# Optimization experiments

Hardware: AMD Instinct MI355X
Metric: run time of the kernel (lower is better)

The kernel has to match this reference:

```python
import jax, jax.numpy as jnp
import numpy as np

N = 100000
E = 1600000
IN_C = 128
OUT_C = 64
EDGE_DIM = 16
EDGE_HID = 32
EPS = 1e-5


def setup_inputs() -> dict:
    key = jax.random.key(0)
    ks = jax.random.split(key, 12)
    x = jax.random.normal(ks[0], (N, IN_C), dtype=jnp.float32)
    edge_index = jax.random.randint(ks[1], (2, E), 0, N, dtype=jnp.int64)
    edge_attr = jax.random.uniform(ks[2], (E, EDGE_DIM), dtype=jnp.float32)
    # PDNConv params
    lin_w = jax.random.normal(ks[3], (OUT_C, IN_C), dtype=jnp.float32) / np.sqrt(IN_C)
    bias = jnp.zeros((OUT_C,), dtype=jnp.float32)
    mlp_w1 = jax.random.normal(ks[4], (EDGE_HID, EDGE_DIM), dtype=jnp.float32) / np.sqrt(EDGE_DIM)
    mlp_b1 = jnp.zeros((EDGE_HID,), dtype=jnp.float32)
    mlp_w2 = jax.random.normal(ks[5], (1, EDGE_HID), dtype=jnp.float32) / np.sqrt(EDGE_HID)
    mlp_b2 = jnp.zeros((1,), dtype=jnp.float32)
    # PReLU (single shared parameter, torch default init 0.25)
    prelu_a = jnp.asarray(0.25, dtype=jnp.float32)
    # GraphNorm params
    gn_weight = jnp.ones((OUT_C,), dtype=jnp.float32)
    gn_bias = jnp.zeros((OUT_C,), dtype=jnp.float32)
    gn_mean_scale = jnp.ones((OUT_C,), dtype=jnp.float32)
    return {
        "x": x, "edge_index": edge_index, "edge_attr": edge_attr,
        "lin_w": lin_w, "bias": bias,
        "mlp_w1": mlp_w1, "mlp_b1": mlp_b1, "mlp_w2": mlp_w2, "mlp_b2": mlp_b2,
        "prelu_a": prelu_a,
        "gn_weight": gn_weight, "gn_bias": gn_bias, "gn_mean_scale": gn_mean_scale,
    }


def reference(x, edge_index, edge_attr, lin_w, bias, mlp_w1, mlp_b1, mlp_w2, mlp_b2,
              prelu_a, gn_weight, gn_bias, gn_mean_scale):
    n = x.shape[0]
    # --- PDNConv ---
    # edge MLP: Linear -> ReLU -> Linear -> Sigmoid -> scalar gate per edge
    h = jax.nn.relu(edge_attr @ mlp_w1.T + mlp_b1)           # [E, hid]
    ew = jax.nn.sigmoid(h @ mlp_w2.T + mlp_b2)[:, 0]         # [E]
    # add self-loops with weight 1.0
    loop = jnp.arange(n)
    row = jnp.concatenate([edge_index[0], loop])             # source
    col = jnp.concatenate([edge_index[1], loop])             # target
    ew = jnp.concatenate([ew, jnp.ones((n,), dtype=x.dtype)])
    # gcn_norm: D^{-1/2} A D^{-1/2} with weighted degree on targets
    deg = jax.ops.segment_sum(ew, col, num_segments=n)       # [N]
    dinv = jnp.where(deg > 0, jax.lax.rsqrt(deg), 0.0)
    norm = dinv[row] * ew * dinv[col]                        # [E+N]
    xt = x @ lin_w.T                                         # [N, out]
    msgs = norm[:, None] * xt[row]                           # gather + gate
    out = jax.ops.segment_sum(msgs, col, num_segments=n) + bias  # scatter-add
    # --- PReLU ---
    out = jnp.where(out >= 0, out, prelu_a * out)
    # --- GraphNorm (single graph) ---
    mean = out.mean(axis=0)                                  # [out]
    centered = out - gn_mean_scale * mean
    var = jnp.mean(centered * centered, axis=0)
    out = gn_weight * centered * jax.lax.rsqrt(var + EPS) + gn_bias
    return out
```

## Files before the change

kernel.cpp:

```cpp
#include <hip/hip_runtime.h>
#include <hip/hip_fp16.h>
#include <math.h>

#define IN_C   128
#define OUT_C  64
#define EDIM   16
#define EHID   32
#define GN_EPS 1e-5f

#define DPAD 3

typedef unsigned long long u64;

__device__ __forceinline__ float dot4(float4 a, float4 b) {
    return a.x * b.x + a.y * b.y + a.z * b.z + a.w * b.w;
}
__device__ __forceinline__ void fma4(float4& a, float s, float4 w) {
    a.x = fmaf(s, w.x, a.x); a.y = fmaf(s, w.y, a.y);
    a.z = fmaf(s, w.z, a.z); a.w = fmaf(s, w.w, a.w);
}
__device__ __forceinline__ float getc(float4 v, int j) {
    return j == 0 ? v.x : j == 1 ? v.y : j == 2 ? v.z : v.w;
}

__global__ void k_init(u64* __restrict__ degcnt, float* __restrict__ sums, int N) {
    int i = blockIdx.x * 256 + threadIdx.x;
    if (i < N) degcnt[(size_t)i << DPAD] = (1ull << 32);
    if (i < 2 * OUT_C) sums[i] = 0.f;
}

__global__ void k_edge(const float* __restrict__ ea, const int* __restrict__ ei,
                       const float* __restrict__ w1, const float* __restrict__ b1,
                       const float* __restrict__ w2, const float* __restrict__ b2,
                       u64* __restrict__ degcnt, int2* __restrict__ tmp, int E) {
    int e = blockIdx.x * 256 + threadIdx.x;
    if (e >= E) return;

    const float4* eav = (const float4*)ea + (size_t)e * 4;
    float4 a0 = eav[0], a1 = eav[1], a2 = eav[2], a3 = eav[3];

    const float4* w1v = (const float4*)w1;
    float z = b2[0];
    #pragma unroll
    for (int j = 0; j < EHID; ++j) {
        float4 q0 = w1v[j * 4 + 0];
        float4 q1 = w1v[j * 4 + 1];
        float4 q2 = w1v[j * 4 + 2];
        float4 q3 = w1v[j * 4 + 3];
        float h = dot4(a0, q0) + dot4(a1, q1) + dot4(a2, q2) + dot4(a3, q3) + b1[j];
        h = fmaxf(h, 0.f);
        z += h * w2[j];
    }
    float ewv = 1.f / (1.f + __expf(-z));

    int row = ei[e];
    int col = ei[E + e];
    u64 inc = (1ull << 44) | (u64)(ewv * 4294967296.0f);
    u64 old = atomicAdd(&degcnt[(size_t)col << DPAD], inc);
    int rank = (int)(old >> 44);
    tmp[e] = make_int2(row | (rank << 17), __float_as_int(ewv));
}

__global__ void k_finish(const u64* __restrict__ degcnt, float* __restrict__ dinv,
                         int* __restrict__ cnt, int N) {
    int i = blockIdx.x * 256 + threadIdx.x;
    if (i < N) {
        u64 v = degcnt[(size_t)i << DPAD];
        float deg = (float)(v & ((1ull << 44) - 1)) * (1.f / 4294967296.f);
        dinv[i] = rsqrtf(deg);
        cnt[i] = (int)(v >> 44);
    }
}

__global__ void k_scan1(const u64* __restrict__ degcnt, int* __restrict__ start,
                        int* __restrict__ bsums, float* __restrict__ dinv,
                        int* __restrict__ cnt, int N) {
    __shared__ int s[256];
    int t = threadIdx.x;
    int i = blockIdx.x * 256 + t;
    int v = 0;
    if (i < N) {
        u64 dv = degcnt[(size_t)i << DPAD];
        v = (int)(dv >> 44);
        float deg = (float)(dv & ((1ull << 44) - 1)) * (1.f / 4294967296.f);
        dinv[i] = rsqrtf(deg);
        cnt[i] = v;
    }
    s[t] = v;
    __syncthreads();
    #pragma unroll
    for (int off = 1; off < 256; off <<= 1) {
        int u = (t >= off) ? s[t - off] : 0;
        __syncthreads();
        s[t] += u;
        __syncthreads();
    }
    if (i < N) start[i] = s[t] - v;
    if (t == 255) bsums[blockIdx.x] = s[255];
}
__global__ void k_scan2(int* __restrict__ bsums, int nb) {
    __shared__ int s[1024];
    int t = threadIdx.x;
    s[t] = (t < nb) ? bsums[t] : 0;
    __syncthreads();
    #pragma unroll
    for (int off = 1; off < 1024; off <<= 1) {
        int u = (t >= off) ? s[t - off] : 0;
        __syncthreads();
        s[t] += u;
        __syncthreads();
    }
    if (t < nb) bsums[t] = (t == 0) ? 0 : s[t - 1];
}

__global__ void k_pass2(const int* __restrict__ ei, const int2* __restrict__ tmp,
                        const int* __restrict__ start, const int* __restrict__ bsums,
                        u64* __restrict__ rec, int E) {
    int e = blockIdx.x * 256 + threadIdx.x;
    if (e >= E) return;
    int col = ei[E + e];
    int2 t = tmp[e];
    int rank = ((unsigned)t.x) >> 17;
    int pos = start[col] + bsums[col >> 8] + rank;
    u64 v = (u64)(unsigned)(t.x & 0x1FFFF) | ((u64)(unsigned)t.y << 32);
    __hip_atomic_store(&rec[pos], v, __ATOMIC_RELAXED, __HIP_MEMORY_SCOPE_AGENT);
}

__global__ void k_xt(const float* __restrict__ x, const float* __restrict__ lw,
                     const float* __restrict__ dinv, __half* __restrict__ xts, int N) {
    __shared__ float swt[IN_C * OUT_C];
    int tid = threadIdx.x;
    for (int i = tid; i < IN_C * OUT_C; i += 256) {
        int k = i >> 6, c = i & 63;
        swt[i] = lw[c * IN_C + k];
    }
    __syncthreads();

    int lane = tid & 63;
    int c4 = lane & 15;
    int rq = lane >> 4;
    int rbase = blockIdx.x * 64 + (tid >> 6) * 16 + rq * 4;

    int r0 = min(rbase + 0, N - 1), r1 = min(rbase + 1, N - 1);
    int r2 = min(rbase + 2, N - 1), r3 = min(rbase + 3, N - 1);
    const float4* x4 = (const float4*)x;
    float4 acc0 = {0,0,0,0}, acc1 = {0,0,0,0}, acc2 = {0,0,0,0}, acc3 = {0,0,0,0};

    #pragma unroll 4
    for (int k4 = 0; k4 < IN_C / 4; ++k4) {
        float4 xv0 = x4[(size_t)r0 * 32 + k4];
        float4 xv1 = x4[(size_t)r1 * 32 + k4];
        float4 xv2 = x4[(size_t)r2 * 32 + k4];
        float4 xv3 = x4[(size_t)r3 * 32 + k4];
        #pragma unroll
        for (int j = 0; j < 4; ++j) {
            float4 wv = *(const float4*)&swt[(k4 * 4 + j) * OUT_C + (c4 << 2)];
            fma4(acc0, getc(xv0, j), wv);
            fma4(acc1, getc(xv1, j), wv);
            fma4(acc2, getc(xv2, j), wv);
            fma4(acc3, getc(xv3, j), wv);
        }
    }
    int cc = c4 << 2;
    #pragma unroll
    for (int i = 0; i < 4; ++i) {
        int r = rbase + i;
        if (r < N) {
            float d = dinv[r];
            float4 a = i == 0 ? acc0 : i == 1 ? acc1 : i == 2 ? acc2 : acc3;
            union { __half2 h[2]; uint2 u; } cv;
            cv.h[0] = __floats2half2_rn(a.x * d, a.y * d);
            cv.h[1] = __floats2half2_rn(a.z * d, a.w * d);
            *(uint2*)&xts[(size_t)r * OUT_C + cc] = cv.u;
        }
    }
}

__global__ void k_gather(const u64* __restrict__ rec, const int* __restrict__ start,
                         const int* __restrict__ bsums, const int* __restrict__ cnt,
                         const float* __restrict__ dinv, const __half* __restrict__ xts,
                         const float* __restrict__ bias, float* __restrict__ out, int N) {
    int node = blockIdx.x * 4 + (threadIdx.x >> 6);
    if (node >= N) return;
    int lane = threadIdx.x & 63;
    int beg = start[node] + bsums[node >> 8];
    int num = cnt[node];
    float acc = __half2float(xts[((size_t)node << 6) + lane]);
    int j = 0;
    for (; j + 8 <= num; j += 8) {
        u64 rc[8];
        #pragma unroll
        for (int u = 0; u < 8; ++u) rc[u] = rec[beg + j + u];
        float v[8];
        #pragma unroll
        for (int u = 0; u < 8; ++u)
            v[u] = __half2float(xts[((size_t)(unsigned)(rc[u] & 0x1FFFF) << 6) + lane]);
        #pragma unroll
        for (int u = 0; u < 8; ++u)
            acc = fmaf(__int_as_float((int)(rc[u] >> 32)), v[u], acc);
    }
    for (; j < num; ++j) {
        u64 rc = rec[beg + j];
        acc = fmaf(__int_as_float((int)(rc >> 32)),
                   __half2float(xts[((size_t)(unsigned)(rc & 0x1FFFF) << 6) + lane]), acc);
    }
    out[((size_t)node << 6) + lane] = bias[lane] + dinv[node] * acc;
}

__global__ void k_init_out(const float* __restrict__ bias, const float* __restrict__ dinv,
                           const __half* __restrict__ xts, float* __restrict__ out, int total) {
    int t = blockIdx.x * 256 + threadIdx.x;
    if (t >= total) return;
    int i = t >> 6, c = t & 63;
    out[t] = bias[c] + dinv[i] * __half2float(xts[t]);
}
__global__ void k_scatter(const int* __restrict__ ei, const int2* __restrict__ tmp,
                          const float* __restrict__ dinv, const __half* __restrict__ xts,
                          float* __restrict__ out, int E) {
    int t = blockIdx.x * 256 + threadIdx.x;
    int e = t >> 6;
    if (e >= E) return;
    int lane = t & 63;
    int2 tm = tmp[e];
    int row = tm.x & 0x1FFFF;
    int col = ei[E + e];
    float w = dinv[col] * __int_as_float(tm.y);
    atomicAdd(out + (size_t)col * OUT_C + lane,
              w * __half2float(xts[(size_t)row * OUT_C + lane]));
}

__global__ void k_stats(const float* __restrict__ out, const float* __restrict__ pa,
                        float* __restrict__ sums, int total) {
    __shared__ float r1[256], r2[256];
    float a = pa[0];
    float s = 0.f, s2 = 0.f;
    int stride = gridDim.x * 256;
    for (int t = blockIdx.x * 256 + threadIdx.x; t < total; t += stride) {
        float v = out[t];
        float y = v >= 0.f ? v : a * v;
        s += y; s2 += y * y;
    }
    int tid = threadIdx.x;
    r1[tid] = s; r2[tid] = s2;
    __syncthreads();
    if (tid < 64) {
        float t1 = r1[tid] + r1[tid + 64] + r1[tid + 128] + r1[tid + 192];
        float t2 = r2[tid] + r2[tid + 64] + r2[tid + 128] + r2[tid + 192];
        atomicAdd(&sums[tid], t1);
        atomicAdd(&sums[OUT_C + tid], t2);
    }
}
__global__ void k_apply(float* __restrict__ out, const float* __restrict__ pa,
                        const float* __restrict__ sums,
                        const float* __restrict__ gw, const float* __restrict__ gb,
                        const float* __restrict__ gms, int total, float invN) {
    int t = blockIdx.x * 256 + threadIdx.x;
    if (t >= total) return;
    int c = t & 63;
    float a  = pa[0];
    float m  = sums[c] * invN;
    float ms = gms[c];
    float var = sums[OUT_C + c] * invN - ms * m * m * (2.f - ms);
    float A = gw[c] * rsqrtf(var + GN_EPS);
    float v = out[t];
    float y = v >= 0.f ? v : a * v;
    out[t] = A * (y - ms * m) + gb[c];
}

extern "C" void kernel_launch(void* const* d_in, const int* in_sizes, int n_in,
                              void* d_out, int out_size, void* d_ws, size_t ws_size,
                              hipStream_t stream) {
    (void)n_in; (void)out_size;
    const float* x    = (const float*)d_in[0];
    const int*   ei   = (const int*)  d_in[1];
    const float* ea   = (const float*)d_in[2];
    const float* lw   = (const float*)d_in[3];
    const float* bias = (const float*)d_in[4];
    const float* w1   = (const float*)d_in[5];
    const float* b1   = (const float*)d_in[6];
    const float* w2   = (const float*)d_in[7];
    const float* b2   = (const float*)d_in[8];
    const float* pa   = (const float*)d_in[9];
    const float* gw   = (const float*)d_in[10];
    const float* gb   = (const float*)d_in[11];
    const float* gms  = (const float*)d_in[12];
    float* out = (float*)d_out;

    int N = in_sizes[0] / IN_C;
    int E = in_sizes[2] / EDIM;
    int total = N * OUT_C;
    int nbN = (N + 255) / 256;
    int nbE = (E + 255) / 256;

    char* p = (char*)d_ws;
    u64*   degcnt = (u64*)p;  p += sizeof(u64) * ((size_t)N << DPAD);
    float* dinv   = (float*)p; p += sizeof(float) * (size_t)N;
    __half* xts   = (__half*)p; p += sizeof(__half) * (size_t)N * OUT_C;
    float* sums   = (float*)p; p += sizeof(float) * 128;
    int*   cnt    = (int*)p;   p += sizeof(int) * (size_t)N;
    int*   startv = (int*)p;   p += sizeof(int) * (size_t)N;
    int*   bsums  = (int*)p;   p += sizeof(int) * 1024;
    int2*  tmp    = (int2*)p;  p += sizeof(int2) * (size_t)E;
    u64*   rec    = (u64*)p;   p += sizeof(u64) * (size_t)E;
    size_t need = (size_t)(p - (char*)d_ws);
    bool use_csr = (need <= ws_size) && (nbN <= 1024);

    k_init <<<nbN, 256, 0, stream>>>(degcnt, sums, N);
    k_edge <<<nbE, 256, 0, stream>>>(ea, ei, w1, b1, w2, b2, degcnt, tmp, E);

    if (use_csr) {
        k_scan1 <<<nbN, 256, 0, stream>>>(degcnt, startv, bsums, dinv, cnt, N);
        k_scan2 <<<1, 1024, 0, stream>>>(bsums, nbN);
        k_pass2 <<<nbE, 256, 0, stream>>>(ei, tmp, startv, bsums, rec, E);
        k_xt    <<<(N + 63) / 64, 256, 0, stream>>>(x, lw, dinv, xts, N);
        k_gather<<<(N + 3) / 4, 256, 0, stream>>>(rec, startv, bsums, cnt, dinv, xts, bias, out, N);
    } else {
        k_finish<<<nbN, 256, 0, stream>>>(degcnt, dinv, cnt, N);
        k_xt    <<<(N + 63) / 64, 256, 0, stream>>>(x, lw, dinv, xts, N);
        k_init_out<<<(total + 255) / 256, 256, 0, stream>>>(bias, dinv, xts, out, total);
        long st = (long)E * 64;
        k_scatter <<<(unsigned)((st + 255) / 256), 256, 0, stream>>>(ei, tmp, dinv, xts, out, E);
    }

    k_stats <<<512, 256, 0, stream>>>(out, pa, sums, total);
    k_apply <<<(total + 255) / 256, 256, 0, stream>>>(out, pa, sums, gw, gb, gms, total,
                                                      1.0f / (float)N);
}
```

Before: 467.2 us.

## Fuse PReLU and GraphNorm statistics into CSR gather kernel; unpad degree counters

The CSR gather kernel becomes grid-stride, applies PReLU, writes the activated output and accumulates per-channel sum and sum-of-squares, which are then atomically added. This removes the separate stats pass, a full re-read of the 25.6MB output, and lets the apply kernel skip PReLU. DPAD drops from 3 to 0, so degree counters are packed rather than spaced out, which shrinks the init and scan footprint but may raise atomic contention between neighbouring counters. Capping the grid at 2048 blocks may reduce latency hiding in the gather.

```diff
diff --git a/kernel.cpp b/kernel.cpp
--- a/kernel.cpp
+++ b/kernel.cpp
@@ -8,7 +8,7 @@
 #define EHID   32
 #define GN_EPS 1e-5f
 
-#define DPAD 3
+#define DPAD 0
 
 typedef unsigned long long u64;
 
@@ -179,32 +179,55 @@
 __global__ void k_gather(const u64* __restrict__ rec, const int* __restrict__ start,
                          const int* __restrict__ bsums, const int* __restrict__ cnt,
                          const float* __restrict__ dinv, const __half* __restrict__ xts,
-                         const float* __restrict__ bias, float* __restrict__ out, int N) {
-    int node = blockIdx.x * 4 + (threadIdx.x >> 6);
-    if (node >= N) return;
-    int lane = threadIdx.x & 63;
-    int beg = start[node] + bsums[node >> 8];
-    int num = cnt[node];
-    float acc = __half2float(xts[((size_t)node << 6) + lane]);
-    int j = 0;
-    for (; j + 8 <= num; j += 8) {
-        u64 rc[8];
-        #pragma unroll
-        for (int u = 0; u < 8; ++u) rc[u] = rec[beg + j + u];
-        float v[8];
-        #pragma unroll
-        for (int u = 0; u < 8; ++u)
-            v[u] = __half2float(xts[((size_t)(unsigned)(rc[u] & 0x1FFFF) << 6) + lane]);
-        #pragma unroll
-        for (int u = 0; u < 8; ++u)
-            acc = fmaf(__int_as_float((int)(rc[u] >> 32)), v[u], acc);
-    }
-    for (; j < num; ++j) {
-        u64 rc = rec[beg + j];
-        acc = fmaf(__int_as_float((int)(rc >> 32)),
-                   __half2float(xts[((size_t)(unsigned)(rc & 0x1FFFF) << 6) + lane]), acc);
-    }
-    out[((size_t)node << 6) + lane] = bias[lane] + dinv[node] * acc;
+                         const float* __restrict__ bias, const float* __restrict__ pa,
+                         float* __restrict__ out, float* __restrict__ sums, int N) {
+    __shared__ float r1[256], r2[256];
+    int tid  = threadIdx.x;
+    int lane = tid & 63;
+    float a = pa[0];
+    float bl = bias[lane];
+    float s = 0.f, s2 = 0.f;
+
+    int ngroups = (N + 3) >> 2;
+    for (int g = blockIdx.x; g < ngroups; g += gridDim.x) {
+        int node = g * 4 + (tid >> 6);
+        if (node < N) {
+            int beg = start[node] + bsums[node >> 8];
+            int num = cnt[node];
+            float acc = __half2float(xts[((size_t)node << 6) + lane]);
+            int j = 0;
+            for (; j + 8 <= num; j += 8) {
+                u64 rc[8];
+                #pragma unroll
+                for (int u = 0; u < 8; ++u) rc[u] = rec[beg + j + u];
+                float v[8];
+                #pragma unroll
+                for (int u = 0; u < 8; ++u)
+                    v[u] = __half2float(xts[((size_t)(unsigned)(rc[u] & 0x1FFFF) << 6) + lane]);
+                #pragma unroll
+                for (int u = 0; u < 8; ++u)
+                    acc = fmaf(__int_as_float((int)(rc[u] >> 32)), v[u], acc);
+            }
+            for (; j < num; ++j) {
+                u64 rc = rec[beg + j];
+                acc = fmaf(__int_as_float((int)(rc >> 32)),
+                           __half2float(xts[((size_t)(unsigned)(rc & 0x1FFFF) << 6) + lane]), acc);
+            }
+            float v = bl + dinv[node] * acc;
+            float y = v >= 0.f ? v : a * v;
+            out[((size_t)node << 6) + lane] = y;
+            s += y; s2 += y * y;
+        }
+    }
+
+    r1[tid] = s; r2[tid] = s2;
+    __syncthreads();
+    if (tid < 64) {
+        float t1 = r1[tid] + r1[tid + 64] + r1[tid + 128] + r1[tid + 192];
+        float t2 = r2[tid] + r2[tid + 64] + r2[tid + 128] + r2[tid + 192];
+        atomicAdd(&sums[tid], t1);
+        atomicAdd(&sums[OUT_C + tid], t2);
+    }
 }
 
 __global__ void k_init_out(const float* __restrict__ bias, const float* __restrict__ dinv,
@@ -228,7 +251,6 @@
     atomicAdd(out + (size_t)col * OUT_C + lane,
               w * __half2float(xts[(size_t)row * OUT_C + lane]));
 }
-
 __global__ void k_stats(const float* __restrict__ out, const float* __restrict__ pa,
                         float* __restrict__ sums, int total) {
     __shared__ float r1[256], r2[256];
@@ -250,10 +272,24 @@
         atomicAdd(&sums[OUT_C + tid], t2);
     }
 }
-__global__ void k_apply(float* __restrict__ out, const float* __restrict__ pa,
-                        const float* __restrict__ sums,
-                        const float* __restrict__ gw, const float* __restrict__ gb,
-                        const float* __restrict__ gms, int total, float invN) {
+
+__global__ void k_apply_csr(float* __restrict__ out, const float* __restrict__ sums,
+                            const float* __restrict__ gw, const float* __restrict__ gb,
+                            const float* __restrict__ gms, int total, float invN) {
+    int t = blockIdx.x * 256 + threadIdx.x;
+    if (t >= total) return;
+    int c = t & 63;
+    float m  = sums[c] * invN;
+    float ms = gms[c];
+    float var = sums[OUT_C + c] * invN - ms * m * m * (2.f - ms);
+    float A = gw[c] * rsqrtf(var + GN_EPS);
+    float y = out[t];
+    out[t] = A * (y - ms * m) + gb[c];
+}
+__global__ void k_apply_fb(float* __restrict__ out, const float* __restrict__ pa,
+                           const float* __restrict__ sums,
+                           const float* __restrict__ gw, const float* __restrict__ gb,
+                           const float* __restrict__ gms, int total, float invN) {
     int t = blockIdx.x * 256 + threadIdx.x;
     if (t >= total) return;
     int c = t & 63;
@@ -309,20 +345,24 @@
     k_edge <<<nbE, 256, 0, stream>>>(ea, ei, w1, b1, w2, b2, degcnt, tmp, E);
 
     if (use_csr) {
+        int ngroups = (N + 3) >> 2;
+        int gblocks = ngroups < 2048 ? ngroups : 2048;
         k_scan1 <<<nbN, 256, 0, stream>>>(degcnt, startv, bsums, dinv, cnt, N);
         k_scan2 <<<1, 1024, 0, stream>>>(bsums, nbN);
         k_pass2 <<<nbE, 256, 0, stream>>>(ei, tmp, startv, bsums, rec, E);
         k_xt    <<<(N + 63) / 64, 256, 0, stream>>>(x, lw, dinv, xts, N);
-        k_gather<<<(N + 3) / 4, 256, 0, stream>>>(rec, startv, bsums, cnt, dinv, xts, bias, out, N);
+        k_gather<<<gblocks, 256, 0, stream>>>(rec, startv, bsums, cnt, dinv, xts,
+                                              bias, pa, out, sums, N);
+        k_apply_csr<<<(total + 255) / 256, 256, 0, stream>>>(out, sums, gw, gb, gms,
+                                                             total, 1.0f / (float)N);
     } else {
         k_finish<<<nbN, 256, 0, stream>>>(degcnt, dinv, cnt, N);
         k_xt    <<<(N + 63) / 64, 256, 0, stream>>>(x, lw, dinv, xts, N);
         k_init_out<<<(total + 255) / 256, 256, 0, stream>>>(bias, dinv, xts, out, total);
         long st = (long)E * 64;
         k_scatter <<<(unsigned)((st + 255) / 256), 256, 0, stream>>>(ei, tmp, dinv, xts, out, E);
-    }
-
-    k_stats <<<512, 256, 0, stream>>>(out, pa, sums, total);
-    k_apply <<<(total + 255) / 256, 256, 0, stream>>>(out, pa, sums, gw, gb, gms, total,
-                                                      1.0f / (float)N);
-}
+        k_stats <<<512, 256, 0, stream>>>(out, pa, sums, total);
+        k_apply_fb<<<(total + 255) / 256, 256, 0, stream>>>(out, pa, sums, gw, gb, gms,
+                                                            total, 1.0f / (float)N);
+    }
+}
```

New measurement: 477.4 us. 2.2% more time.

## Replace scan-based CSR build with fixed-capacity per-node buckets plus overflow list

Applied to the files above, without the earlier changes.

Instead of counting ranks, prefix-scanning degrees and running a second pass to place edge records, each edge now writes its record straight into a per-node bucket of fixed capacity during the edge-MLP kernel, using the atomic rank. Edges past the capacity go to a small overflow list that a separate kernel scatters with atomics. This removes the two scan kernels and the pass2 kernel along with the tmp buffer round trip. The degree counters also lose their padding. The cost is a sparse, larger record array and a correctness risk if the overflow list exceeds its capacity.

```diff
diff --git a/kernel.cpp b/kernel.cpp
--- a/kernel.cpp
+++ b/kernel.cpp
@@ -7,8 +7,8 @@
 #define EDIM   16
 #define EHID   32
 #define GN_EPS 1e-5f
-
-#define DPAD 3
+#define MAXDEG 48
+#define OVFCAP 2048
 
 typedef unsigned long long u64;
 
@@ -23,16 +23,19 @@
     return j == 0 ? v.x : j == 1 ? v.y : j == 2 ? v.z : v.w;
 }
 
-__global__ void k_init(u64* __restrict__ degcnt, float* __restrict__ sums, int N) {
+__global__ void k_init(u64* __restrict__ degcnt, float* __restrict__ sums,
+                       u64* __restrict__ ovfcnt, int N) {
     int i = blockIdx.x * 256 + threadIdx.x;
-    if (i < N) degcnt[(size_t)i << DPAD] = (1ull << 32);
+    if (i < N) degcnt[i] = (1ull << 32);
     if (i < 2 * OUT_C) sums[i] = 0.f;
+    if (i == 0) *ovfcnt = 0ull;
 }
 
 __global__ void k_edge(const float* __restrict__ ea, const int* __restrict__ ei,
                        const float* __restrict__ w1, const float* __restrict__ b1,
                        const float* __restrict__ w2, const float* __restrict__ b2,
-                       u64* __restrict__ degcnt, int2* __restrict__ tmp, int E) {
+                       u64* __restrict__ degcnt, u64* __restrict__ rec,
+                       u64* __restrict__ ovfcnt, int4* __restrict__ ovflist, int E) {
     int e = blockIdx.x * 256 + threadIdx.x;
     if (e >= E) return;
 
@@ -56,7 +59,43 @@
     int row = ei[e];
     int col = ei[E + e];
     u64 inc = (1ull << 44) | (u64)(ewv * 4294967296.0f);
-    u64 old = atomicAdd(&degcnt[(size_t)col << DPAD], inc);
+    u64 old = atomicAdd(&degcnt[col], inc);
+    int rank = (int)(old >> 44);
+    if (rank < MAXDEG) {
+        u64 v = (u64)(unsigned)row | ((u64)(unsigned)__float_as_int(ewv) << 32);
+        __hip_atomic_store(&rec[(size_t)col * MAXDEG + rank], v,
+                           __ATOMIC_RELAXED, __HIP_MEMORY_SCOPE_AGENT);
+    } else {
+        u64 oi = atomicAdd(ovfcnt, 1ull);
+        if (oi < OVFCAP) ovflist[oi] = make_int4(row, col, __float_as_int(ewv), 0);
+    }
+}
+
+__global__ void k_edge_fb(const float* __restrict__ ea, const int* __restrict__ ei,
+                          const float* __restrict__ w1, const float* __restrict__ b1,
+                          const float* __restrict__ w2, const float* __restrict__ b2,
+                          u64* __restrict__ degcnt, int2* __restrict__ tmp, int E) {
+    int e = blockIdx.x * 256 + threadIdx.x;
+    if (e >= E) return;
+    const float4* eav = (const float4*)ea + (size_t)e * 4;
+    float4 a0 = eav[0], a1 = eav[1], a2 = eav[2], a3 = eav[3];
+    const float4* w1v = (const float4*)w1;
+    float z = b2[0];
+    #pragma unroll
+    for (int j = 0; j < EHID; ++j) {
+        float4 q0 = w1v[j * 4 + 0];
+        float4 q1 = w1v[j * 4 + 1];
+        float4 q2 = w1v[j * 4 + 2];
+        float4 q3 = w1v[j * 4 + 3];
+        float h = dot4(a0, q0) + dot4(a1, q1) + dot4(a2, q2) + dot4(a3, q3) + b1[j];
+        h = fmaxf(h, 0.f);
+        z += h * w2[j];
+    }
+    float ewv = 1.f / (1.f + __expf(-z));
+    int row = ei[e];
+    int col = ei[E + e];
+    u64 inc = (1ull << 44) | (u64)(ewv * 4294967296.0f);
+    u64 old = atomicAdd(&degcnt[col], inc);
     int rank = (int)(old >> 44);
     tmp[e] = make_int2(row | (rank << 17), __float_as_int(ewv));
 }
@@ -65,65 +104,12 @@
                          int* __restrict__ cnt, int N) {
     int i = blockIdx.x * 256 + threadIdx.x;
     if (i < N) {
-        u64 v = degcnt[(size_t)i << DPAD];
+        u64 v = degcnt[i];
         float deg = (float)(v & ((1ull << 44) - 1)) * (1.f / 4294967296.f);
         dinv[i] = rsqrtf(deg);
-        cnt[i] = (int)(v >> 44);
-    }
-}
-
-__global__ void k_scan1(const u64* __restrict__ degcnt, int* __restrict__ start,
-                        int* __restrict__ bsums, float* __restrict__ dinv,
-                        int* __restrict__ cnt, int N) {
-    __shared__ int s[256];
-    int t = threadIdx.x;
-    int i = blockIdx.x * 256 + t;
-    int v = 0;
-    if (i < N) {
-        u64 dv = degcnt[(size_t)i << DPAD];
-        v = (int)(dv >> 44);
-        float deg = (float)(dv & ((1ull << 44) - 1)) * (1.f / 4294967296.f);
-        dinv[i] = rsqrtf(deg);
-        cnt[i] = v;
-    }
-    s[t] = v;
-    __syncthreads();
-    #pragma unroll
-    for (int off = 1; off < 256; off <<= 1) {
-        int u = (t >= off) ? s[t - off] : 0;
-        __syncthreads();
-        s[t] += u;
-        __syncthreads();
-    }
-    if (i < N) start[i] = s[t] - v;
-    if (t == 255) bsums[blockIdx.x] = s[255];
-}
-__global__ void k_scan2(int* __restrict__ bsums, int nb) {
-    __shared__ int s[1024];
-    int t = threadIdx.x;
-    s[t] = (t < nb) ? bsums[t] : 0;
-    __syncthreads();
-    #pragma unroll
-    for (int off = 1; off < 1024; off <<= 1) {
-        int u = (t >= off) ? s[t - off] : 0;
-        __syncthreads();
-        s[t] += u;
-        __syncthreads();
-    }
-    if (t < nb) bsums[t] = (t == 0) ? 0 : s[t - 1];
-}
-
-__global__ void k_pass2(const int* __restrict__ ei, const int2* __restrict__ tmp,
-                        const int* __restrict__ start, const int* __restrict__ bsums,
-                        u64* __restrict__ rec, int E) {
-    int e = blockIdx.x * 256 + threadIdx.x;
-    if (e >= E) return;
-    int col = ei[E + e];
-    int2 t = tmp[e];
-    int rank = ((unsigned)t.x) >> 17;
-    int pos = start[col] + bsums[col >> 8] + rank;
-    u64 v = (u64)(unsigned)(t.x & 0x1FFFF) | ((u64)(unsigned)t.y << 32);
-    __hip_atomic_store(&rec[pos], v, __ATOMIC_RELAXED, __HIP_MEMORY_SCOPE_AGENT);
+        int c = (int)(v >> 44);
+        cnt[i] = c < MAXDEG ? c : MAXDEG;
+    }
 }
 
 __global__ void k_xt(const float* __restrict__ x, const float* __restrict__ lw,
@@ -176,14 +162,13 @@
     }
 }
 
-__global__ void k_gather(const u64* __restrict__ rec, const int* __restrict__ start,
-                         const int* __restrict__ bsums, const int* __restrict__ cnt,
+__global__ void k_gather(const u64* __restrict__ rec, const int* __restrict__ cnt,
                          const float* __restrict__ dinv, const __half* __restrict__ xts,
                          const float* __restrict__ bias, float* __restrict__ out, int N) {
     int node = blockIdx.x * 4 + (threadIdx.x >> 6);
     if (node >= N) return;
     int lane = threadIdx.x & 63;
-    int beg = start[node] + bsums[node >> 8];
+    int beg = node * MAXDEG;
     int num = cnt[node];
     float acc = __half2float(xts[((size_t)node << 6) + lane]);
     int j = 0;
@@ -205,6 +190,20 @@
                    __half2float(xts[((size_t)(unsigned)(rc & 0x1FFFF) << 6) + lane]), acc);
     }
     out[((size_t)node << 6) + lane] = bias[lane] + dinv[node] * acc;
+}
+
+__global__ void k_ovf(const int4* __restrict__ ovflist, const u64* __restrict__ ovfcnt,
+                      const float* __restrict__ dinv, const __half* __restrict__ xts,
+                      float* __restrict__ out) {
+    u64 nv = *ovfcnt;
+    int n = nv > (u64)OVFCAP ? OVFCAP : (int)nv;
+    int lane = threadIdx.x & 63;
+    for (int i = blockIdx.x * 4 + (threadIdx.x >> 6); i < n; i += gridDim.x * 4) {
+        int4 v = ovflist[i];
+        float w = dinv[v.y] * __int_as_float(v.z);
+        atomicAdd(&out[(size_t)v.y * OUT_C + lane],
+                  w * __half2float(xts[(size_t)v.x * OUT_C + lane]));
+    }
 }
 
 __global__ void k_init_out(const float* __restrict__ bias, const float* __restrict__ dinv,
@@ -293,36 +292,42 @@
     int nbE = (E + 255) / 256;
 
     char* p = (char*)d_ws;
-    u64*   degcnt = (u64*)p;  p += sizeof(u64) * ((size_t)N << DPAD);
+    u64*   degcnt = (u64*)p;  p += sizeof(u64) * (size_t)N;
     float* dinv   = (float*)p; p += sizeof(float) * (size_t)N;
     __half* xts   = (__half*)p; p += sizeof(__half) * (size_t)N * OUT_C;
     float* sums   = (float*)p; p += sizeof(float) * 128;
     int*   cnt    = (int*)p;   p += sizeof(int) * (size_t)N;
-    int*   startv = (int*)p;   p += sizeof(int) * (size_t)N;
-    int*   bsums  = (int*)p;   p += sizeof(int) * 1024;
-    int2*  tmp    = (int2*)p;  p += sizeof(int2) * (size_t)E;
-    u64*   rec    = (u64*)p;   p += sizeof(u64) * (size_t)E;
-    size_t need = (size_t)(p - (char*)d_ws);
-    bool use_csr = (need <= ws_size) && (nbN <= 1024);
-
-    k_init <<<nbN, 256, 0, stream>>>(degcnt, sums, N);
-    k_edge <<<nbE, 256, 0, stream>>>(ea, ei, w1, b1, w2, b2, degcnt, tmp, E);
+    char*  tail = p;
+    u64*   ovfcnt  = (u64*)tail;
+    int4*  ovflist = (int4*)(tail + sizeof(u64) * 2);
+    u64*   rec     = (u64*)(tail + sizeof(u64) * 2 + sizeof(int4) * OVFCAP);
+    size_t need_csr = (size_t)((char*)(rec + (size_t)N * MAXDEG) - (char*)d_ws);
+    int2*  tmp = (int2*)tail;
+    size_t need_fb = (size_t)((char*)(tmp + (size_t)E) - (char*)d_ws);
+    bool use_csr = (need_csr <= ws_size) && (N < (1 << 17));
 
     if (use_csr) {
-        k_scan1 <<<nbN, 256, 0, stream>>>(degcnt, startv, bsums, dinv, cnt, N);
-        k_scan2 <<<1, 1024, 0, stream>>>(bsums, nbN);
-        k_pass2 <<<nbE, 256, 0, stream>>>(ei, tmp, startv, bsums, rec, E);
-        k_xt    <<<(N + 63) / 64, 256, 0, stream>>>(x, lw, dinv, xts, N);
-        k_gather<<<(N + 3) / 4, 256, 0, stream>>>(rec, startv, bsums, cnt, dinv, xts, bias, out, N);
-    } else {
+        k_init  <<<nbN, 256, 0, stream>>>(degcnt, sums, ovfcnt, N);
+        k_edge  <<<nbE, 256, 0, stream>>>(ea, ei, w1, b1, w2, b2, degcnt,
+                                          rec, ovfcnt, ovflist, E);
         k_finish<<<nbN, 256, 0, stream>>>(degcnt, dinv, cnt, N);
         k_xt    <<<(N + 63) / 64, 256, 0, stream>>>(x, lw, dinv, xts, N);
+        k_gather<<<(N + 3) / 4, 256, 0, stream>>>(rec, cnt, dinv, xts, bias, out, N);
+        k_ovf   <<<64, 256, 0, stream>>>(ovflist, ovfcnt, dinv, xts, out);
+        k_stats <<<512, 256, 0, stream>>>(out, pa, sums, total);
+        k_apply <<<(total + 255) / 256, 256, 0, stream>>>(out, pa, sums, gw, gb, gms,
+                                                          total, 1.0f / (float)N);
+    } else {
+        (void)need_fb;
+        k_init   <<<nbN, 256, 0, stream>>>(degcnt, sums, (u64*)sums , N);
+        k_edge_fb<<<nbE, 256, 0, stream>>>(ea, ei, w1, b1, w2, b2, degcnt, tmp, E);
+        k_finish <<<nbN, 256, 0, stream>>>(degcnt, dinv, cnt, N);
+        k_xt     <<<(N + 63) / 64, 256, 0, stream>>>(x, lw, dinv, xts, N);
         k_init_out<<<(total + 255) / 256, 256, 0, stream>>>(bias, dinv, xts, out, total);
         long st = (long)E * 64;
         k_scatter <<<(unsigned)((st + 255) / 256), 256, 0, stream>>>(ei, tmp, dinv, xts, out, E);
-    }
-
-    k_stats <<<512, 256, 0, stream>>>(out, pa, sums, total);
-    k_apply <<<(total + 255) / 256, 256, 0, stream>>>(out, pa, sums, gw, gb, gms, total,
-                                                      1.0f / (float)N);
-}
+        k_stats  <<<512, 256, 0, stream>>>(out, pa, sums, total);
+        k_apply  <<<(total + 255) / 256, 256, 0, stream>>>(out, pa, sums, gw, gb, gms,
+                                                           total, 1.0f / (float)N);
+    }
+}
```

Result: faster. 449.1 us (-3.9%).
